# Kernel tuning notes

Hardware: AMD Instinct MI355X
Metric: run time of the kernel (lower is better)

## Reference

```python
import jax, jax.numpy as jnp
import numpy as np

B, T, N, C = 8, 12, 325, 64
S_ORDER, T_ORDER, LAYERS = 10, 5, 2
SKIP, END, OUT_W = 128, 256, 12
EPS = 1e-5


def _fro(x):
    return jnp.sqrt(jnp.sum(x * x, axis=(2, 3), keepdims=True))


def _unit(x):
    return x / jnp.maximum(_fro(x), 1e-8)


def _basis_s(Ls, last, second):
    r = jnp.einsum('nm,bcmt->bcnt', Ls, last)
    r = r - jnp.sum(r * last, axis=(2, 3), keepdims=True) * last
    r = r - jnp.sum(r * second, axis=(2, 3), keepdims=True) * second
    return _unit(r)


def _basis_t(Lt, last, second):
    r = jnp.einsum('bcnt,tu->bcnu', last, Lt)
    r = r - jnp.sum(r * last, axis=(2, 3), keepdims=True) * last
    r = r - jnp.sum(r * second, axis=(2, 3), keepdims=True) * second
    return _unit(r)


def _matrix_list(m00, Ls, Lt):
    # Gram-Schmidt-like 2D orthogonal polynomial recursion; (P+1)*(Q+1) terms
    M = [m00]
    last_s, sec_s = m00, jnp.zeros_like(m00)
    last_t, sec_t = m00, jnp.zeros_like(m00)
    for i in range(S_ORDER + 1):
        if i > 0:
            mi0 = _basis_s(Ls, last_s, sec_s)
            sec_s, last_s = last_s, mi0
            M.append(mi0)
            last_t, sec_t = mi0, jnp.zeros_like(mi0)
        for _ in range(T_ORDER):
            mij = _basis_t(Lt, last_t, sec_t)
            sec_t, last_t = last_t, mij
            M.append(mij)
    return jnp.stack(M, axis=1)  # [B, R, C, N, T]


def _c1x1(x, w, b):
    return jnp.einsum('bint,oi->bont', x, w) + b[None, :, None, None]


def _bn(x, g, b, m, v):
    s = g / jnp.sqrt(v + EPS)
    return (x - m[None, :, None, None]) * s[None, :, None, None] + b[None, :, None, None]


def _gate(y):
    return jax.nn.sigmoid(y[:, :C]) * jnp.tanh(y[:, C:])


def setup_inputs() -> dict:
    key = jax.random.key(0)
    ks = iter(jax.random.split(key, 80))

    def nrm(*shape):
        return jax.random.normal(next(ks), shape, jnp.float32) * 0.1

    def pos(*shape):
        return jax.random.uniform(next(ks), shape, jnp.float32, 0.5, 1.5)

    P1, Q1 = S_ORDER + 1, T_ORDER + 1
    # normalized symmetric spatial matrix  D^-1/2 A D^-1/2
    A = jax.random.uniform(next(ks), (N, N), jnp.float32)
    A = (A + A.T) * 0.5 + jnp.eye(N)
    d = 1.0 / jnp.sqrt(A.sum(0))
    sp_matrix = A * d[:, None] * d[None, :]
    # normalized tridiagonal temporal matrix (as in __init__)
    Tp = jnp.eye(T, k=1) + jnp.eye(T, k=-1)
    dt = 1.0 / jnp.sqrt(Tp.sum(0))
    tp_matrix = Tp * dt[:, None] * dt[None, :]
    return dict(
        source=jax.random.normal(next(ks), (B, T, N, 1), jnp.float32),
        TE=jax.random.randint(next(ks), (B, T, 2), 0, 288, jnp.int32),
        sp_matrix=sp_matrix, tp_matrix=tp_matrix,
        SE=nrm(N, 10),
        tmlp1_w=nrm(S_ORDER, 295), tmlp1_b=nrm(S_ORDER),
        tmlp2_w=nrm(T_ORDER, T), tmlp2_b=nrm(T_ORDER),
        smlp1_w=nrm(T_ORDER, N), smlp1_b=nrm(T_ORDER),
        smlp2_w=nrm(S_ORDER, 10), smlp2_b=nrm(S_ORDER),
        start_w=nrm(C, 1), start_b=nrm(C),
        theta1_w=nrm(LAYERS, Q1, T_ORDER), theta1_b=nrm(LAYERS, Q1),
        theta2_w=nrm(LAYERS, P1, S_ORDER), theta2_b=nrm(LAYERS, P1),
        st_mlp_w=nrm(LAYERS, C, 2 * C), st_mlp_b=nrm(LAYERS, C),
        st_bn_g=pos(LAYERS, C), st_bn_b=nrm(LAYERS, C), st_bn_m=nrm(LAYERS, C), st_bn_v=pos(LAYERS, C),
        pyr1_w=nrm(LAYERS, 2 * C, C), pyr1_b=nrm(LAYERS, 2 * C),
        pyr2_w=nrm(LAYERS, 2 * C, C, 3), pyr2_b=nrm(LAYERS, 2 * C),
        pyr3_w=nrm(LAYERS, 2 * C, C, 6), pyr3_b=nrm(LAYERS, 2 * C),
        pyr_conv_w=nrm(LAYERS, C, 3 * C), pyr_conv_b=nrm(LAYERS, C),
        pyr_bn_g=pos(LAYERS, C), pyr_bn_b=nrm(LAYERS, C), pyr_bn_m=nrm(LAYERS, C), pyr_bn_v=pos(LAYERS, C),
        skip_w=nrm(LAYERS, SKIP, C), skip_b=nrm(LAYERS, SKIP),
        bn_g=pos(LAYERS, C), bn_b=nrm(LAYERS, C), bn_m=nrm(LAYERS, C), bn_v=pos(LAYERS, C),
        end1_w=nrm(END, SKIP), end1_b=nrm(END),
        end2_w=nrm(OUT_W, END), end2_b=nrm(OUT_W),
    )


def reference(source, TE, sp_matrix, tp_matrix, SE, tmlp1_w, tmlp1_b, tmlp2_w, tmlp2_b,
              smlp1_w, smlp1_b, smlp2_w, smlp2_b, start_w, start_b,
              theta1_w, theta1_b, theta2_w, theta2_b, st_mlp_w, st_mlp_b,
              st_bn_g, st_bn_b, st_bn_m, st_bn_v,
              pyr1_w, pyr1_b, pyr2_w, pyr2_b, pyr3_w, pyr3_b,
              pyr_conv_w, pyr_conv_b, pyr_bn_g, pyr_bn_b, pyr_bn_m, pyr_bn_v,
              skip_w, skip_b, bn_g, bn_b, bn_m, bn_v,
              end1_w, end1_b, end2_w, end2_b):
    b = source.shape[0]
    # ---- STEmbedding ----
    dow = jax.nn.one_hot(TE[..., 0] % 7, 7, dtype=jnp.float32)
    tod = jax.nn.one_hot(TE[..., 1] % 288, 288, dtype=jnp.float32)
    te = jnp.concatenate([dow, tod], axis=-1)                                           # [B,T,295]
    te = jax.nn.relu(jnp.einsum('blc,oc->bol', te, tmlp1_w) + tmlp1_b[None, :, None])   # [B,s_order,T]
    te = jax.nn.relu(jnp.einsum('bst,ot->bos', te, tmlp2_w) + tmlp2_b[None, :, None])   # [B,t_order,s_order]
    se = jax.nn.relu(smlp1_w @ SE + smlp1_b[:, None])                                   # [t_order,10]
    se = jax.nn.relu((smlp2_w @ se.T + smlp2_b[:, None]).T)                             # [t_order,s_order]
    ste = jax.nn.relu(se[None] + te)
    # ---- start conv ----
    x = _c1x1(jnp.transpose(source, (0, 3, 2, 1)), start_w, start_b)                    # [B,C,N,T]
    skip = jnp.zeros((b, SKIP, N, T), jnp.float32)
    for i in range(LAYERS):
        residual = x
        # learned coefficients theta: [B,(t_order+1)*(s_order+1)]
        th = jnp.einsum('bts,ot->bos', ste, theta1_w[i]) + theta1_b[i][None, :, None]   # [B,t+1,s]
        th = jnp.einsum('bts,os->bot', th, theta2_w[i]) + theta2_b[i][None, :, None]    # [B,s+1,t+1]
        theta = jax.nn.relu(jnp.transpose(th, (0, 2, 1))).reshape(b, -1)
        # spectral basis recursion + einsum fusion
        m00 = _unit(residual)
        M = _matrix_list(m00, sp_matrix, tp_matrix)
        x_st = jnp.einsum('br,brcnt->bcnt', theta, M)
        hidden = _bn(_c1x1(jnp.concatenate([residual, x_st], axis=1), st_mlp_w[i], st_mlp_b[i]),
                     st_bn_g[i], st_bn_b[i], st_bn_m[i], st_bn_v[i])
        # pyramid temporal conv (gated)
        x1 = _gate(_c1x1(hidden, pyr1_w[i], pyr1_b[i]))
        h2 = hidden.reshape(b, C, N, T // 3, 3)
        x2 = _gate(jnp.einsum('bcnqk,ock->bonq', h2, pyr2_w[i]) + pyr2_b[i][None, :, None, None])
        h3 = hidden.reshape(b, C, N, T // 6, 6)
        x3 = _gate(jnp.einsum('bcnqk,ock->bonq', h3, pyr3_w[i]) + pyr3_b[i][None, :, None, None])
        x2 = jax.image.resize(x2, x1.shape, method='bilinear')
        x3 = jax.image.resize(x3, x1.shape, method='bilinear')
        fusion = _bn(_c1x1(jnp.concatenate([x1, x2, x3], axis=1), pyr_conv_w[i], pyr_conv_b[i]),
                     pyr_bn_g[i], pyr_bn_b[i], pyr_bn_m[i], pyr_bn_v[i])
        skip = skip + _c1x1(fusion, skip_w[i], skip_b[i])
        x = _bn(fusion + residual, bn_g[i], bn_b[i], bn_m[i], bn_v[i])
    out = jax.nn.relu(skip[:, :, :, -1:])
    out = jax.nn.relu(_c1x1(out, end1_w, end1_b))
    out = _c1x1(out, end2_w, end2_b)
    return out  # [B, output_window, N, 1]
```

## Files before the change

kernel.cpp:

```cpp
#include <hip/hip_runtime.h>
#include <hip/hip_bf16.h>
#include <math.h>

#define B_   8
#define T_   12
#define N_   325
#define C_   64
#define NT   3900
#define NTILE 21
#define NKK   11
#define NTHIRD 109

typedef __attribute__((ext_vector_type(8))) short short8v;
typedef __attribute__((ext_vector_type(4))) float f32x4;

__device__ __forceinline__ float sigm(float x) { return 1.f / (1.f + expf(-x)); }

__device__ __forceinline__ unsigned short f2bf(float f) {
  unsigned u = __float_as_uint(f);
  u += 0x7FFF + ((u >> 16) & 1);
  return (unsigned short)(u >> 16);
}
__device__ __forceinline__ float bf2f(unsigned short h) {
  return __uint_as_float(((unsigned)h) << 16);
}

__device__ __forceinline__ void redN(float* v, int nv, float (*redb)[4], int tid) {
#pragma unroll
  for (int off = 1; off < 64; off <<= 1) {
    for (int i = 0; i < nv; i++) v[i] += __shfl_xor(v[i], off, 64);
  }
  if ((tid & 63) == 0) {
    for (int i = 0; i < nv; i++) redb[tid >> 6][i] = v[i];
  }
  __syncthreads();
  for (int i = 0; i < nv; i++) {
    float s = 0.f;
#pragma unroll
    for (int w = 0; w < 8; w++) s += redb[w][i];
    v[i] = s;
  }
}

__device__ __forceinline__ void cvtB(const float* sbp, short8v* bfh0, short8v* bfl0,
                                     int ckbase, int ccc, bool cvalid, int cobase) {
  unsigned short* dh = (unsigned short*)bfh0;
  unsigned short* dl = (unsigned short*)bfl0;
#pragma unroll
  for (int kk = 0; kk < NKK; kk++) {
    int k = kk * 32 + ckbase;
    float v = (cvalid && k < N_) ? sbp[k * 12 + ccc] : 0.f;
    unsigned short h = f2bf(v);
    dh[kk * 512 + cobase] = h;
    dl[kk * 512 + cobase] = f2bf(v - bf2f(h));
  }
}

__global__ __launch_bounds__(256) void k_sentinel(float* out, int n) {
  int i = blockIdx.x * 256 + threadIdx.x;
  if (i < n) out[i] = 7.0f;
}

__global__ __launch_bounds__(256) void k0_frag(const float* __restrict__ sp,
                                               unsigned short* __restrict__ fragA) {
  int idx = blockIdx.x * 256 + threadIdx.x;
  if (idx >= NTILE * NKK * 64) return;
  int lane = idx & 63, tk = idx >> 6;
  int row = (tk / NKK) * 16 + (lane & 15);
  int k0 = (tk % NKK) * 32 + (lane >> 4) * 8;
  size_t base = ((size_t)tk * 2) * 512 + (size_t)lane * 8;
#pragma unroll
  for (int j = 0; j < 8; j++) {
    int k = k0 + j;
    float v = (row < N_ && k < N_) ? sp[row * N_ + k] : 0.f;
    unsigned short h = f2bf(v);
    fragA[base + j] = h;
    fragA[base + 512 + j] = f2bf(v - bf2f(h));
  }
}

__global__ __launch_bounds__(256) void k1_embed(
    const int* __restrict__ TE, const float* __restrict__ SE,
    const float* __restrict__ w1, const float* __restrict__ b1,
    const float* __restrict__ w2, const float* __restrict__ b2,
    const float* __restrict__ sw1, const float* __restrict__ sb1,
    const float* __restrict__ sw2, const float* __restrict__ sb2,
    const float* __restrict__ t1w, const float* __restrict__ t1b,
    const float* __restrict__ t2w, const float* __restrict__ t2b,
    float* __restrict__ coef) {
  __shared__ float te2[8][10][12];
  __shared__ float ste[8][5][10];
  __shared__ float se1[5][10];
  __shared__ float se2[5][10];
  __shared__ float th[8][6][10];
  __shared__ int te64;
  const int tid = threadIdx.x;
  if (tid == 0) {
    int nz = 0;
    for (int k2 = 0; k2 < 96; k2++) nz += (TE[2 * k2 + 1] != 0) ? 1 : 0;
    te64 = (nz == 0) ? 1 : 0;
  }
  __syncthreads();
  for (int idx = tid; idx < 960; idx += 256) {
    int t = idx % 12, o = (idx / 12) % 10, b = idx / 120;
    int q = (b * 12 + t) * 2;
    int d = (te64 ? TE[2 * q] : TE[q]) % 7;
    int h = (te64 ? TE[2 * q + 2] : TE[q + 1]) % 288;
    float v = w1[o * 295 + d] + w1[o * 295 + 7 + h] + b1[o];
    te2[b][o][t] = fmaxf(v, 0.f);
  }
  __syncthreads();
  for (int idx = tid; idx < 400; idx += 256) {
    int s = idx % 10, o = (idx / 10) % 5, b = idx / 50;
    float a = b2[o];
    for (int t = 0; t < 12; t++) a += te2[b][s][t] * w2[o * 12 + t];
    ste[b][o][s] = fmaxf(a, 0.f);
  }
  if (tid < 50) {
    int o = tid / 10, j = tid % 10;
    float a = sb1[o];
    for (int n = 0; n < N_; n++) a += sw1[o * N_ + n] * SE[n * 10 + j];
    se1[o][j] = fmaxf(a, 0.f);
  }
  __syncthreads();
  if (tid < 50) {
    int t = tid / 10, s = tid % 10;
    float a = sb2[s];
    for (int j = 0; j < 10; j++) a += sw2[s * 10 + j] * se1[t][j];
    se2[t][s] = fmaxf(a, 0.f);
  }
  __syncthreads();
  for (int idx = tid; idx < 400; idx += 256) {
    int s = idx % 10, o = (idx / 10) % 5, b = idx / 50;
    ste[b][o][s] = fmaxf(se2[o][s] + ste[b][o][s], 0.f);
  }
  __syncthreads();
  for (int l = 0; l < 2; l++) {
    for (int idx = tid; idx < 480; idx += 256) {
      int s = idx % 10, q = (idx / 10) % 6, b = idx / 60;
      float a = t1b[l * 6 + q];
      for (int t = 0; t < 5; t++) a += ste[b][t][s] * t1w[(l * 6 + q) * 5 + t];
      th[b][q][s] = a;
    }
    __syncthreads();
    for (int idx = tid; idx < 528; idx += 256) {
      int q = idx % 6, p = (idx / 6) % 11, b = idx / 66;
      float a = t2b[l * 11 + p];
      for (int s = 0; s < 10; s++) a += th[b][q][s] * t2w[(l * 11 + p) * 10 + s];
      coef[(l * 8 + b) * 66 + q * 11 + p] = fmaxf(a, 0.f);
    }
    __syncthreads();
  }
}

__global__ __launch_bounds__(256) void k2_start(const float* __restrict__ src,
                                                const float* __restrict__ w,
                                                const float* __restrict__ bia,
                                                float* __restrict__ x) {
  int idx = blockIdx.x * 256 + threadIdx.x;
  if (idx >= B_ * C_ * NT) return;
  int pos = idx % NT, r = idx / NT, c = r & 63, b = r >> 6;
  int n = pos / 12, t = pos - 12 * n;
  float s = src[(b * 12 + t) * N_ + n];
  x[idx] = s * w[c] + bia[c];
}

__global__ __launch_bounds__(512)
__attribute__((amdgpu_waves_per_eu(4, 4))) void k3_basis(
    const float* __restrict__ x, const unsigned short* __restrict__ fragA,
    const float* __restrict__ tp, const float* __restrict__ coef,
    float* __restrict__ xst) {
  __shared__ float sb[2][3940];
  __shared__ float rbuf[3936];
  __shared__ float sred[2][8][4];
  __shared__ short8v bfh0[704];
  __shared__ short8v bfl0[704];
  const int tid = threadIdx.x;
  const int bc = blockIdx.x;
  const float* cf = coef + (bc >> 6) * 66;
  const float* xs = x + (size_t)bc * NT;
  float* xo = xst + (size_t)bc * NT;

  const int wv = tid >> 6, lane = tid & 63;
  const int ccol = lane & 15, krow = lane >> 4;

  const int cj = tid & 7, ccc = (tid >> 3) & 15, ckr = (tid >> 7) & 3;
  const int ckbase = ckr * 8 + cj;
  const bool cvalid = (ccc < 12);
  const int cobase = (ckr * 16 + ccc) * 8 + cj;

  const bool upd = tid < 246;
  const int rq = tid / 3, tq = tid - 3 * (tid / 3);
  const int e0 = rq * 4 * 12 + tq * 4;

  const bool actT = (tid < N_);
  const int rowOff = tid * 12;

  float w[11];
#pragma unroll
  for (int k = 0; k < 11; k++) w[k] = tp[k * 12 + k + 1];

  float last[12], sec[12], acc[12];
  int p = 0, m = 0, spc = 0;

  if (tid < 80) {
    int bsel = tid / 40, off = tid - 40 * bsel;
    sb[bsel][3900 + off] = 0.f;
  }

  {
    float np = 0.f;
#pragma unroll
    for (int u = 0; u < 12; u++) last[u] = 0.f;
    if (actT) {
      const float4 a = *(const float4*)(xs + rowOff);
      const float4 b4 = *(const float4*)(xs + rowOff + 4);
      const float4 c4 = *(const float4*)(xs + rowOff + 8);
      last[0] = a.x; last[1] = a.y; last[2] = a.z; last[3] = a.w;
      last[4] = b4.x; last[5] = b4.y; last[6] = b4.z; last[7] = b4.w;
      last[8] = c4.x; last[9] = c4.y; last[10] = c4.z; last[11] = c4.w;
#pragma unroll
      for (int u = 0; u < 12; u++) np += last[u] * last[u];
    }
    p ^= 1; redN(&np, 1, sred[p], tid);
    const float inv = 1.f / fmaxf(sqrtf(np), 1e-8f);
    const float c0 = cf[m]; m++;
#pragma unroll
    for (int u = 0; u < 12; u++) {
      last[u] *= inv;
      acc[u] = c0 * last[u];
      sec[u] = 0.f;
    }
    if (actT) {
      float4 wv4;
      wv4.x = last[0]; wv4.y = last[1]; wv4.z = last[2]; wv4.w = last[3];
      *(float4*)&sb[0][rowOff] = wv4;
      wv4.x = last[4]; wv4.y = last[5]; wv4.z = last[6]; wv4.w = last[7];
      *(float4*)&sb[0][rowOff + 4] = wv4;
      wv4.x = last[8]; wv4.y = last[9]; wv4.z = last[10]; wv4.w = last[11];
      *(float4*)&sb[0][rowOff + 8] = wv4;
    }
    __syncthreads();
    cvtB(sb[0], bfh0, bfl0, ckbase, ccc, cvalid, cobase);
  }

  for (int i = 0; i <= 10; i++) {
    if (i > 0) {
      const int sps = 1 - spc;
      const bool hasSec = (i >= 2);
#pragma unroll 1
      for (int g = 0; g < 3; g++) {
        const int tile = wv + g * 8;
        if (tile < NTILE) {
          f32x4 cc = {0.f, 0.f, 0.f, 0.f};
#pragma unroll 1
          for (int kk = 0; kk < NKK; kk++) {
            const short8v bh = bfh0[kk * 64 + lane];
            const short8v bl = bfl0[kk * 64 + lane];
            const short8v* pa = (const short8v*)fragA +
                                ((size_t)(tile * NKK + kk) * 2) * 64 + lane;
            short8v ah = pa[0], al = pa[64];
            cc = __builtin_amdgcn_mfma_f32_16x16x32_bf16(ah, bh, cc, 0, 0, 0);
            cc = __builtin_amdgcn_mfma_f32_16x16x32_bf16(ah, bl, cc, 0, 0, 0);
            cc = __builtin_amdgcn_mfma_f32_16x16x32_bf16(al, bh, cc, 0, 0, 0);
          }
          if (ccol < 12) {
#pragma unroll
            for (int r = 0; r < 4; r++) {
              int row = tile * 16 + krow * 4 + r;
              if (row < 328) rbuf[row * 12 + ccol] = cc[r];
            }
          }
        }
      }
      __syncthreads();
      float rt[4][4];
      float v4[4] = {0.f, 0.f, 0.f, 0.f};
      if (upd) {
#pragma unroll
        for (int ii = 0; ii < 4; ii++) {
          const float4 q = *(const float4*)&rbuf[e0 + ii * 12];
          rt[ii][0] = q.x; rt[ii][1] = q.y; rt[ii][2] = q.z; rt[ii][3] = q.w;
          const float4 lq = *(const float4*)&sb[spc][e0 + ii * 12];
          v4[0] += rt[ii][0] * lq.x + rt[ii][1] * lq.y + rt[ii][2] * lq.z + rt[ii][3] * lq.w;
          v4[3] += rt[ii][0] * rt[ii][0] + rt[ii][1] * rt[ii][1] +
                   rt[ii][2] * rt[ii][2] + rt[ii][3] * rt[ii][3];
          if (hasSec) {
            const float4 sq4 = *(const float4*)&sb[sps][e0 + ii * 12];
            v4[1] += rt[ii][0] * sq4.x + rt[ii][1] * sq4.y + rt[ii][2] * sq4.z + rt[ii][3] * sq4.w;
            v4[2] += lq.x * sq4.x + lq.y * sq4.y + lq.z * sq4.z + lq.w * sq4.w;
          }
        }
      }
      p ^= 1; redN(v4, 4, sred[p], tid);
      const float d1 = v4[0];
      const float d2 = hasSec ? (v4[1] - d1 * v4[2]) : 0.f;
      const float np = fmaxf(v4[3] - d1 * d1 - d2 * d2, 0.f);
      const float inv = 1.f / fmaxf(sqrtf(np), 1e-8f);
      const float cs = cf[m]; m++;
      if (upd) {
#pragma unroll
        for (int ii = 0; ii < 4; ii++) {
          const float4 lq = *(const float4*)&sb[spc][e0 + ii * 12];
          float sx = 0.f, sy = 0.f, sz = 0.f, sw = 0.f;
          if (hasSec) {
            const float4 sq4 = *(const float4*)&sb[sps][e0 + ii * 12];
            sx = sq4.x; sy = sq4.y; sz = sq4.z; sw = sq4.w;
          }
          float4 wv4;
          wv4.x = (rt[ii][0] - d1 * lq.x - d2 * sx) * inv;
          wv4.y = (rt[ii][1] - d1 * lq.y - d2 * sy) * inv;
          wv4.z = (rt[ii][2] - d1 * lq.z - d2 * sz) * inv;
          wv4.w = (rt[ii][3] - d1 * lq.w - d2 * sw) * inv;
          *(float4*)&sb[sps][e0 + ii * 12] = wv4;
        }
      }
      spc = sps;
      __syncthreads();
      if (i < 10) cvtB(sb[spc], bfh0, bfl0, ckbase, ccc, cvalid, cobase);
      if (actT) {
        const float4 a = *(const float4*)&sb[spc][rowOff];
        const float4 b4 = *(const float4*)&sb[spc][rowOff + 4];
        const float4 c4 = *(const float4*)&sb[spc][rowOff + 8];
        last[0] = a.x; last[1] = a.y; last[2] = a.z; last[3] = a.w;
        last[4] = b4.x; last[5] = b4.y; last[6] = b4.z; last[7] = b4.w;
        last[8] = c4.x; last[9] = c4.y; last[10] = c4.z; last[11] = c4.w;
#pragma unroll
        for (int u = 0; u < 12; u++) {
          acc[u] += cs * last[u];
          sec[u] = 0.f;
        }
      }
    }
    for (int j5 = 0; j5 < 5; j5++) {
      float v4[4] = {0.f, 0.f, 0.f, 0.f};
      if (actT) {
#pragma unroll
        for (int u = 0; u < 12; u++) {
          float r = 0.f;
          if (u > 0) r += last[u - 1] * w[u - 1];
          if (u < 11) r += last[u + 1] * w[u];
          v4[0] += r * last[u];
          v4[1] += r * sec[u];
          v4[2] += last[u] * sec[u];
          v4[3] += r * r;
        }
      }
      p ^= 1; redN(v4, 4, sred[p], tid);
      const float d1 = v4[0];
      const float d2 = v4[1] - d1 * v4[2];
      const float np = fmaxf(v4[3] - d1 * d1 - d2 * d2, 0.f);
      const float inv = 1.f / fmaxf(sqrtf(np), 1e-8f);
      const float c = cf[m]; m++;
      if (actT) {
        float pm1 = 0.f;
#pragma unroll
        for (int u = 0; u < 12; u++) {
          const float tmp = last[u];
          float r = 0.f;
          if (u > 0) r += pm1 * w[u - 1];
          if (u < 11) r += last[u + 1] * w[u];
          const float v = (r - d1 * tmp - d2 * sec[u]) * inv;
          acc[u] += c * v;
          sec[u] = tmp;
          last[u] = v;
          pm1 = tmp;
        }
      }
    }
  }
  if (actT) {
    float4 wv4;
    wv4.x = acc[0]; wv4.y = acc[1]; wv4.z = acc[2]; wv4.w = acc[3];
    *(float4*)(xo + rowOff) = wv4;
    wv4.x = acc[4]; wv4.y = acc[5]; wv4.z = acc[6]; wv4.w = acc[7];
    *(float4*)(xo + rowOff + 4) = wv4;
    wv4.x = acc[8]; wv4.y = acc[9]; wv4.z = acc[10]; wv4.w = acc[11];
    *(float4*)(xo + rowOff + 8) = wv4;
  }
}

__global__ __launch_bounds__(256) void k45_layer(
    float* __restrict__ x, const float* __restrict__ xst,
    const float* __restrict__ stw, const float* __restrict__ stb,
    const float* __restrict__ stg, const float* __restrict__ stbb,
    const float* __restrict__ stm, const float* __restrict__ stv,
    const float* __restrict__ p1w, const float* __restrict__ p1b,
    const float* __restrict__ p2w, const float* __restrict__ p2b,
    const float* __restrict__ p3w, const float* __restrict__ p3b,
    const float* __restrict__ pcw, const float* __restrict__ pcb,
    const float* __restrict__ pbg, const float* __restrict__ pbb,
    const float* __restrict__ pbm, const float* __restrict__ pbv,
    const float* __restrict__ bng, const float* __restrict__ bnb,
    const float* __restrict__ bnm, const float* __restrict__ bnv,
    const float* __restrict__ skw, const float* __restrict__ skb,
    float* __restrict__ skipb, int accum) {
  __shared__ float xr[3][64][12];
  __shared__ float xq_g1s[3][64][12];
  __shared__ float hd[3][64][12];
  __shared__ float g2s[3][64][4];
  __shared__ float g3s[3][64][2];
  __shared__ float fu11[3][64];
  float (*xq)[64][12] = xq_g1s;
  float (*g1s)[64][12] = xq_g1s;
  const int tid = threadIdx.x;
  const int bid = blockIdx.x;
  const int b = bid / NTHIRD, nn = bid - NTHIRD * b;
  const int n0 = nn * 3;
  const bool val1 = (n0 + 1 < N_), val2 = (n0 + 2 < N_);
  const size_t base0 = ((size_t)b * 64) * NT + n0 * 12;
  if (tid < 192) {
    int c = tid / 3, ch = tid - 3 * (tid / 3);
    *(float4*)&xr[0][c][ch * 4] = *(const float4*)(x + base0 + (size_t)c * NT + ch * 4);
    *(float4*)&xq[0][c][ch * 4] = *(const float4*)(xst + base0 + (size_t)c * NT + ch * 4);
    float4 z = {0.f, 0.f, 0.f, 0.f};
    if (val1) {
      *(float4*)&xr[1][c][ch * 4] = *(const float4*)(x + base0 + 12 + (size_t)c * NT + ch * 4);
      *(float4*)&xq[1][c][ch * 4] = *(const float4*)(xst + base0 + 12 + (size_t)c * NT + ch * 4);
    } else {
      *(float4*)&xr[1][c][ch * 4] = z;
      *(float4*)&xq[1][c][ch * 4] = z;
    }
    if (val2) {
      *(float4*)&xr[2][c][ch * 4] = *(const float4*)(x + base0 + 24 + (size_t)c * NT + ch * 4);
      *(float4*)&xq[2][c][ch * 4] = *(const float4*)(xst + base0 + 24 + (size_t)c * NT + ch * 4);
    } else {
      *(float4*)&xr[2][c][ch * 4] = z;
      *(float4*)&xq[2][c][ch * 4] = z;
    }
  }
  __syncthreads();
  if (tid < 192) {
    int oq = tid / 12, t = tid - 12 * (tid / 12);
    float a[3][4] = {{0.f}};
    const float* w0 = stw + (4 * oq) * 128;
    for (int i = 0; i < 64; i++) {
      float wa = w0[i], wb = w0[128 + i], wc = w0[256 + i], wd = w0[384 + i];
#pragma unroll
      for (int s = 0; s < 3; s++) {
        float h = xr[s][i][t];
        a[s][0] += h * wa; a[s][1] += h * wb; a[s][2] += h * wc; a[s][3] += h * wd;
      }
    }
    for (int i = 0; i < 64; i++) {
      float wa = w0[64 + i], wb = w0[192 + i], wc = w0[320 + i], wd = w0[448 + i];
#pragma unroll
      for (int s = 0; s < 3; s++) {
        float h = xq[s][i][t];
        a[s][0] += h * wa; a[s][1] += h * wb; a[s][2] += h * wc; a[s][3] += h * wd;
      }
    }
#pragma unroll
    for (int k = 0; k < 4; k++) {
      int o = 4 * oq + k;
      float sc = stg[o] / sqrtf(stv[o] + 1e-5f);
#pragma unroll
      for (int s = 0; s < 3; s++)
        hd[s][o][t] = (a[s][k] + stb[o] - stm[o]) * sc + stbb[o];
    }
  }
  __syncthreads();
  if (tid < 192) {
    int oq = tid / 12, t = tid - 12 * (tid / 12);
    float sa[3][4] = {{0.f}}, ua[3][4] = {{0.f}};
    const float* wsr = p1w + (4 * oq) * 64;
    for (int i = 0; i < 64; i++) {
      float wa = wsr[i], wb = wsr[64 + i], wc = wsr[128 + i], wd = wsr[192 + i];
      float va = wsr[4096 + i], vb = wsr[4096 + 64 + i];
      float vc = wsr[4096 + 128 + i], vd = wsr[4096 + 192 + i];
#pragma unroll
      for (int s = 0; s < 3; s++) {
        float h = hd[s][i][t];
        sa[s][0] += h * wa; sa[s][1] += h * wb; sa[s][2] += h * wc; sa[s][3] += h * wd;
        ua[s][0] += h * va; ua[s][1] += h * vb; ua[s][2] += h * vc; ua[s][3] += h * vd;
      }
    }
#pragma unroll
    for (int k = 0; k < 4; k++) {
      int o = 4 * oq + k;
#pragma unroll
      for (int s = 0; s < 3; s++)
        g1s[s][o][t] = sigm(sa[s][k] + p1b[o]) * tanhf(ua[s][k] + p1b[o + 64]);
    }
  }
  if (tid < 128) {
    int oq = tid / 4, q = tid & 3;
    float sa[3][2] = {{0.f}}, ua[3][2] = {{0.f}};
    const float* wsr = p2w + (2 * oq) * 192;
    for (int i = 0; i < 64; i++)
#pragma unroll
      for (int kk = 0; kk < 3; kk++) {
        float wa = wsr[i * 3 + kk], wb = wsr[192 + i * 3 + kk];
        float va = wsr[12288 + i * 3 + kk], vb = wsr[12288 + 192 + i * 3 + kk];
#pragma unroll
        for (int s = 0; s < 3; s++) {
          float h = hd[s][i][3 * q + kk];
          sa[s][0] += h * wa; sa[s][1] += h * wb;
          ua[s][0] += h * va; ua[s][1] += h * vb;
        }
      }
    int o = 2 * oq;
#pragma unroll
    for (int s = 0; s < 3; s++) {
      g2s[s][o][q] = sigm(sa[s][0] + p2b[o]) * tanhf(ua[s][0] + p2b[o + 64]);
      g2s[s][o + 1][q] = sigm(sa[s][1] + p2b[o + 1]) * tanhf(ua[s][1] + p2b[o + 65]);
    }
  } else if (tid < 192) {
    int r = tid - 128;
    int oq = r / 2, q = r & 1;
    float sa[3][2] = {{0.f}}, ua[3][2] = {{0.f}};
    const float* wsr = p3w + (2 * oq) * 384;
    for (int i = 0; i < 64; i++)
#pragma unroll
      for (int kk = 0; kk < 6; kk++) {
        float wa = wsr[i * 6 + kk], wb = wsr[384 + i * 6 + kk];
        float va = wsr[24576 + i * 6 + kk], vb = wsr[24576 + 384 + i * 6 + kk];
#pragma unroll
        for (int s = 0; s < 3; s++) {
          float h = hd[s][i][6 * q + kk];
          sa[s][0] += h * wa; sa[s][1] += h * wb;
          ua[s][0] += h * va; ua[s][1] += h * vb;
        }
      }
    int o = 2 * oq;
#pragma unroll
    for (int s = 0; s < 3; s++) {
      g3s[s][o][q] = sigm(sa[s][0] + p3b[o]) * tanhf(ua[s][0] + p3b[o + 64]);
      g3s[s][o + 1][q] = sigm(sa[s][1] + p3b[o + 1]) * tanhf(ua[s][1] + p3b[o + 65]);
    }
  }
  __syncthreads();
  if (tid < 192) {
    int oq = tid / 12, t = tid - 12 * (tid / 12);
    float a[3][4] = {{0.f}};
    const float* w0 = pcw + (4 * oq) * 192;
    for (int c = 0; c < 64; c++) {
      float wa = w0[c], wb = w0[192 + c], wc = w0[384 + c], wd = w0[576 + c];
#pragma unroll
      for (int s = 0; s < 3; s++) {
        float v = g1s[s][c][t];
        a[s][0] += v * wa; a[s][1] += v * wb; a[s][2] += v * wc; a[s][3] += v * wd;
      }
    }
    float c4 = fminf(fmaxf((t - 1) * (1.f / 3.f), 0.f), 3.f);
    int q0 = (int)c4;
    float f4 = c4 - (float)q0;
    int q1 = min(q0 + 1, 3);
    for (int c = 0; c < 64; c++) {
      float wa = w0[64 + c], wb = w0[192 + 64 + c], wc = w0[384 + 64 + c], wd = w0[576 + 64 + c];
#pragma unroll
      for (int s = 0; s < 3; s++) {
        float v = (1.f - f4) * g2s[s][c][q0] + f4 * g2s[s][c][q1];
        a[s][0] += v * wa; a[s][1] += v * wb; a[s][2] += v * wc; a[s][3] += v * wd;
      }
    }
    float f2 = fminf(fmaxf((2 * t - 5) * (1.f / 12.f), 0.f), 1.f);
    for (int c = 0; c < 64; c++) {
      float wa = w0[128 + c], wb = w0[192 + 128 + c], wc = w0[384 + 128 + c], wd = w0[576 + 128 + c];
#pragma unroll
      for (int s = 0; s < 3; s++) {
        float v = (1.f - f2) * g3s[s][c][0] + f2 * g3s[s][c][1];
        a[s][0] += v * wa; a[s][1] += v * wb; a[s][2] += v * wc; a[s][3] += v * wd;
      }
    }
#pragma unroll
    for (int k = 0; k < 4; k++) {
      int o = 4 * oq + k;
      float s1 = pbg[o] / sqrtf(pbv[o] + 1e-5f);
      float s2 = bng[o] / sqrtf(bnv[o] + 1e-5f);
#pragma unroll
      for (int s = 0; s < 3; s++) {
        float fv = (a[s][k] + pcb[o] - pbm[o]) * s1 + pbb[o];
        if (t == 11) fu11[s][o] = fv;
        xr[s][o][t] = (fv + xr[s][o][t] - bnm[o]) * s2 + bnb[o];
      }
    }
  }
  __syncthreads();
  if (tid < 192) {
    int c = tid / 3, ch = tid - 3 * (tid / 3);
    *(float4*)(x + base0 + (size_t)c * NT + ch * 4) = *(float4*)&xr[0][c][ch * 4];
    if (val1)
      *(float4*)(x + base0 + 12 + (size_t)c * NT + ch * 4) = *(float4*)&xr[1][c][ch * 4];
    if (val2)
      *(float4*)(x + base0 + 24 + (size_t)c * NT + ch * 4) = *(float4*)&xr[2][c][ch * 4];
  }
  if (tid < 128) {
    float a[3];
    a[0] = skb[tid]; a[1] = skb[tid]; a[2] = skb[tid];
    const float* wr = skw + tid * 64;
    for (int c = 0; c < 64; c++) {
      float wv = wr[c];
#pragma unroll
      for (int s = 0; s < 3; s++) a[s] += fu11[s][c] * wv;
    }
    size_t o0 = ((size_t)b * 128 + tid) * N_ + n0;
    skipb[o0] = accum ? (skipb[o0] + a[0]) : a[0];
    if (val1) skipb[o0 + 1] = accum ? (skipb[o0 + 1] + a[1]) : a[1];
    if (val2) skipb[o0 + 2] = accum ? (skipb[o0 + 2] + a[2]) : a[2];
  }
}

__global__ __launch_bounds__(256) void k6_end(const float* __restrict__ skip,
                                              const float* __restrict__ w1,
                                              const float* __restrict__ b1,
                                              const float* __restrict__ w2,
                                              const float* __restrict__ b2,
                                              float* __restrict__ out) {
  __shared__ float sk[128];
  __shared__ float h[256];
  const int blk = blockIdx.x;
  const int b = blk / N_;
  const int n = blk - N_ * b;
  const int tid = threadIdx.x;
  if (tid < 128) sk[tid] = fmaxf(skip[((size_t)b * 128 + tid) * N_ + n], 0.f);
  __syncthreads();
  {
    float a = b1[tid];
    for (int s = 0; s < 128; s++) a += w1[tid * 128 + s] * sk[s];
    h[tid] = fmaxf(a, 0.f);
  }
  __syncthreads();
  if (tid < 12) {
    float a = b2[tid];
    for (int e = 0; e < 256; e++) a += w2[tid * 256 + e] * h[e];
    out[((size_t)b * 12 + tid) * N_ + n] = a;
  }
}

extern "C" void kernel_launch(void* const* d_in, const int* in_sizes, int n_in,
                              void* d_out, int out_size, void* d_ws, size_t ws_size,
                              hipStream_t stream) {
  (void)in_sizes; (void)n_in;
  if (ws_size < (size_t)44 * 1024 * 1024) {
    k_sentinel<<<(out_size + 255) / 256, 256, 0, stream>>>((float*)d_out, out_size);
    return;
  }
  const float* src = (const float*)d_in[0];
  const int* TE = (const int*)d_in[1];
  const float* sp = (const float*)d_in[2];
  const float* tp = (const float*)d_in[3];
  const float* SE = (const float*)d_in[4];
  const float* tmlp1_w = (const float*)d_in[5];
  const float* tmlp1_b = (const float*)d_in[6];
  const float* tmlp2_w = (const float*)d_in[7];
  const float* tmlp2_b = (const float*)d_in[8];
  const float* smlp1_w = (const float*)d_in[9];
  const float* smlp1_b = (const float*)d_in[10];
  const float* smlp2_w = (const float*)d_in[11];
  const float* smlp2_b = (const float*)d_in[12];
  const float* start_w = (const float*)d_in[13];
  const float* start_b = (const float*)d_in[14];
  const float* th1w = (const float*)d_in[15];
  const float* th1b = (const float*)d_in[16];
  const float* th2w = (const float*)d_in[17];
  const float* th2b = (const float*)d_in[18];
  const float* stw = (const float*)d_in[19];
  const float* stb = (const float*)d_in[20];
  const float* stg = (const float*)d_in[21];
  const float* stbb = (const float*)d_in[22];
  const float* stm = (const float*)d_in[23];
  const float* stv = (const float*)d_in[24];
  const float* p1w = (const float*)d_in[25];
  const float* p1b = (const float*)d_in[26];
  const float* p2w = (const float*)d_in[27];
  const float* p2b = (const float*)d_in[28];
  const float* p3w = (const float*)d_in[29];
  const float* p3b = (const float*)d_in[30];
  const float* pcw = (const float*)d_in[31];
  const float* pcb = (const float*)d_in[32];
  const float* pbg = (const float*)d_in[33];
  const float* pbb = (const float*)d_in[34];
  const float* pbm = (const float*)d_in[35];
  const float* pbv = (const float*)d_in[36];
  const float* skw = (const float*)d_in[37];
  const float* skb = (const float*)d_in[38];
  const float* bng = (const float*)d_in[39];
  const float* bnb = (const float*)d_in[40];
  const float* bnm = (const float*)d_in[41];
  const float* bnv = (const float*)d_in[42];
  const float* e1w = (const float*)d_in[43];
  const float* e1b = (const float*)d_in[44];
  const float* e2w = (const float*)d_in[45];
  const float* e2b = (const float*)d_in[46];

  float* ws = (float*)d_ws;
  float* coef = ws + 0;
  unsigned short* fragA = (unsigned short*)(ws + 8192);
  float* x    = ws + 4194304;
  float* xst  = ws + 6291456;
  float* skipb= ws + 10485760;

  k0_frag<<<(NTILE * NKK * 64 + 255) / 256, 256, 0, stream>>>(sp, fragA);
  k1_embed<<<1, 256, 0, stream>>>(TE, SE, tmlp1_w, tmlp1_b, tmlp2_w, tmlp2_b,
                                  smlp1_w, smlp1_b, smlp2_w, smlp2_b,
                                  th1w, th1b, th2w, th2b, coef);
  k2_start<<<(B_ * C_ * NT + 255) / 256, 256, 0, stream>>>(src, start_w, start_b, x);

  for (int l = 0; l < 2; l++) {
    k3_basis<<<512, 512, 0, stream>>>(x, fragA, tp, coef + l * 528, xst);
    k45_layer<<<B_ * NTHIRD, 256, 0, stream>>>(
        x, xst,
        stw + l * 8192, stb + l * 64, stg + l * 64, stbb + l * 64,
        stm + l * 64, stv + l * 64,
        p1w + l * 8192, p1b + l * 128,
        p2w + l * 24576, p2b + l * 128,
        p3w + l * 49152, p3b + l * 128,
        pcw + l * 12288, pcb + l * 64,
        pbg + l * 64, pbb + l * 64, pbm + l * 64, pbv + l * 64,
        bng + l * 64, bnb + l * 64, bnm + l * 64, bnv + l * 64,
        skw + l * 8192, skb + l * 128,
        skipb, l);
  }
  k6_end<<<B_ * N_, 256, 0, stream>>>(skipb, e1w, e1b, e2w, e2b, (float*)d_out);
}
```

Measured before the change: 899.6 us.

## Fuse front-end kernels into one launch and end MLP into final layer kernel

Merges the start convolution, spatial-matrix fragment preparation and embedding MLP into a single kernel dispatched by block index. It also folds the final ReLU/end MLP into the last layer kernel so the accumulated skip is consumed directly instead of being written and re-read. The aim is to cut kernel launch gaps and a global skip round trip. The cost is a larger per-block shared footprint and extra per-block work in the layer kernel.

Result: faster. 831.5 us (median of 2 runs) (-7.6%).

```diff
diff --git a/kernel.cpp b/kernel.cpp
--- a/kernel.cpp
+++ b/kernel.cpp
@@ -10,6 +10,7 @@
 #define NTILE 21
 #define NKK   11
 #define NTHIRD 109
+#define K2BLK 7800
 
 typedef __attribute__((ext_vector_type(8))) short short8v;
 typedef __attribute__((ext_vector_type(4))) float f32x4;
@@ -61,25 +62,10 @@
   if (i < n) out[i] = 7.0f;
 }
 
-__global__ __launch_bounds__(256) void k0_frag(const float* __restrict__ sp,
-                                               unsigned short* __restrict__ fragA) {
-  int idx = blockIdx.x * 256 + threadIdx.x;
-  if (idx >= NTILE * NKK * 64) return;
-  int lane = idx & 63, tk = idx >> 6;
-  int row = (tk / NKK) * 16 + (lane & 15);
-  int k0 = (tk % NKK) * 32 + (lane >> 4) * 8;
-  size_t base = ((size_t)tk * 2) * 512 + (size_t)lane * 8;
-#pragma unroll
-  for (int j = 0; j < 8; j++) {
-    int k = k0 + j;
-    float v = (row < N_ && k < N_) ? sp[row * N_ + k] : 0.f;
-    unsigned short h = f2bf(v);
-    fragA[base + j] = h;
-    fragA[base + 512 + j] = f2bf(v - bf2f(h));
-  }
-}
-
-__global__ __launch_bounds__(256) void k1_embed(
+__global__ __launch_bounds__(256) void k012_front(
+    const float* __restrict__ src, const float* __restrict__ cw,
+    const float* __restrict__ cbia, float* __restrict__ x,
+    const float* __restrict__ sp, unsigned short* __restrict__ fragA,
     const int* __restrict__ TE, const float* __restrict__ SE,
     const float* __restrict__ w1, const float* __restrict__ b1,
     const float* __restrict__ w2, const float* __restrict__ b2,
@@ -95,6 +81,31 @@
   __shared__ float th[8][6][10];
   __shared__ int te64;
   const int tid = threadIdx.x;
+  const int blk = blockIdx.x;
+  if (blk < K2BLK) {
+    int idx = blk * 256 + tid;
+    int pos = idx % NT, r = idx / NT, c = r & 63, b = r >> 6;
+    int n = pos / 12, t = pos - 12 * n;
+    float s = src[(b * 12 + t) * N_ + n];
+    x[idx] = s * cw[c] + cbia[c];
+    return;
+  } else if (blk > K2BLK) {
+    int idx = (blk - K2BLK - 1) * 256 + tid;
+    if (idx >= NTILE * NKK * 64) return;
+    int lane = idx & 63, tk = idx >> 6;
+    int row = (tk / NKK) * 16 + (lane & 15);
+    int k0 = (tk % NKK) * 32 + (lane >> 4) * 8;
+    size_t base = ((size_t)tk * 2) * 512 + (size_t)lane * 8;
+#pragma unroll
+    for (int j = 0; j < 8; j++) {
+      int k = k0 + j;
+      float v = (row < N_ && k < N_) ? sp[row * N_ + k] : 0.f;
+      unsigned short h = f2bf(v);
+      fragA[base + j] = h;
+      fragA[base + 512 + j] = f2bf(v - bf2f(h));
+    }
+    return;
+  }
   if (tid == 0) {
     int nz = 0;
     for (int k2 = 0; k2 < 96; k2++) nz += (TE[2 * k2 + 1] != 0) ? 1 : 0;
@@ -151,18 +162,6 @@
     }
     __syncthreads();
   }
-}
-
-__global__ __launch_bounds__(256) void k2_start(const float* __restrict__ src,
-                                                const float* __restrict__ w,
-                                                const float* __restrict__ bia,
-                                                float* __restrict__ x) {
-  int idx = blockIdx.x * 256 + threadIdx.x;
-  if (idx >= B_ * C_ * NT) return;
-  int pos = idx % NT, r = idx / NT, c = r & 63, b = r >> 6;
-  int n = pos / 12, t = pos - 12 * n;
-  float s = src[(b * 12 + t) * N_ + n];
-  x[idx] = s * w[c] + bia[c];
 }
 
 __global__ __launch_bounds__(512)
@@ -394,13 +393,18 @@
     const float* __restrict__ bng, const float* __restrict__ bnb,
     const float* __restrict__ bnm, const float* __restrict__ bnv,
     const float* __restrict__ skw, const float* __restrict__ skb,
-    float* __restrict__ skipb, int accum) {
+    float* __restrict__ skipb, int accum,
+    const float* __restrict__ e1w, const float* __restrict__ e1b,
+    const float* __restrict__ e2w, const float* __restrict__ e2b,
+    float* __restrict__ out) {
   __shared__ float xr[3][64][12];
   __shared__ float xq_g1s[3][64][12];
   __shared__ float hd[3][64][12];
   __shared__ float g2s[3][64][4];
   __shared__ float g3s[3][64][2];
   __shared__ float fu11[3][64];
+  __shared__ float sk2[3][128];
+  __shared__ float h2[3][256];
   float (*xq)[64][12] = xq_g1s;
   float (*g1s)[64][12] = xq_g1s;
   const int tid = threadIdx.x;
@@ -595,36 +599,41 @@
       for (int s = 0; s < 3; s++) a[s] += fu11[s][c] * wv;
     }
     size_t o0 = ((size_t)b * 128 + tid) * N_ + n0;
-    skipb[o0] = accum ? (skipb[o0] + a[0]) : a[0];
-    if (val1) skipb[o0 + 1] = accum ? (skipb[o0 + 1] + a[1]) : a[1];
-    if (val2) skipb[o0 + 2] = accum ? (skipb[o0 + 2] + a[2]) : a[2];
-  }
-}
-
-__global__ __launch_bounds__(256) void k6_end(const float* __restrict__ skip,
-                                              const float* __restrict__ w1,
-                                              const float* __restrict__ b1,
-                                              const float* __restrict__ w2,
-                                              const float* __restrict__ b2,
-                                              float* __restrict__ out) {
-  __shared__ float sk[128];
-  __shared__ float h[256];
-  const int blk = blockIdx.x;
-  const int b = blk / N_;
-  const int n = blk - N_ * b;
-  const int tid = threadIdx.x;
-  if (tid < 128) sk[tid] = fmaxf(skip[((size_t)b * 128 + tid) * N_ + n], 0.f);
-  __syncthreads();
-  {
-    float a = b1[tid];
-    for (int s = 0; s < 128; s++) a += w1[tid * 128 + s] * sk[s];
-    h[tid] = fmaxf(a, 0.f);
-  }
-  __syncthreads();
-  if (tid < 12) {
-    float a = b2[tid];
-    for (int e = 0; e < 256; e++) a += w2[tid * 256 + e] * h[e];
-    out[((size_t)b * 12 + tid) * N_ + n] = a;
+    if (accum) {
+      sk2[0][tid] = fmaxf(skipb[o0] + a[0], 0.f);
+      sk2[1][tid] = val1 ? fmaxf(skipb[o0 + 1] + a[1], 0.f) : 0.f;
+      sk2[2][tid] = val2 ? fmaxf(skipb[o0 + 2] + a[2], 0.f) : 0.f;
+    } else {
+      skipb[o0] = a[0];
+      if (val1) skipb[o0 + 1] = a[1];
+      if (val2) skipb[o0 + 2] = a[2];
+    }
+  }
+  if (accum) {
+    __syncthreads();
+    {
+      float a1[3];
+      a1[0] = e1b[tid]; a1[1] = a1[0]; a1[2] = a1[0];
+      const float* wr1 = e1w + tid * 128;
+      for (int ss = 0; ss < 128; ss++) {
+        float wv = wr1[ss];
+#pragma unroll
+        for (int s = 0; s < 3; s++) a1[s] += wv * sk2[s][ss];
+      }
+#pragma unroll
+      for (int s = 0; s < 3; s++) h2[s][tid] = fmaxf(a1[s], 0.f);
+    }
+    __syncthreads();
+    if (tid < 36) {
+      int s = tid / 12, tt = tid - 12 * (tid / 12);
+      bool ok = (s == 0) || (s == 1 && val1) || (s == 2 && val2);
+      if (ok) {
+        float a2 = e2b[tt];
+        const float* wr2 = e2w + tt * 256;
+        for (int e = 0; e < 256; e++) a2 += wr2[e] * h2[s][e];
+        out[((size_t)b * 12 + tt) * N_ + n0 + s] = a2;
+      }
+    }
   }
 }
 
@@ -691,11 +700,12 @@
   float* xst  = ws + 6291456;
   float* skipb= ws + 10485760;
 
-  k0_frag<<<(NTILE * NKK * 64 + 255) / 256, 256, 0, stream>>>(sp, fragA);
-  k1_embed<<<1, 256, 0, stream>>>(TE, SE, tmlp1_w, tmlp1_b, tmlp2_w, tmlp2_b,
-                                  smlp1_w, smlp1_b, smlp2_w, smlp2_b,
-                                  th1w, th1b, th2w, th2b, coef);
-  k2_start<<<(B_ * C_ * NT + 255) / 256, 256, 0, stream>>>(src, start_w, start_b, x);
+  const int k0blks = (NTILE * NKK * 64 + 255) / 256;
+  k012_front<<<K2BLK + 1 + k0blks, 256, 0, stream>>>(
+      src, start_w, start_b, x, sp, fragA,
+      TE, SE, tmlp1_w, tmlp1_b, tmlp2_w, tmlp2_b,
+      smlp1_w, smlp1_b, smlp2_w, smlp2_b,
+      th1w, th1b, th2w, th2b, coef);
 
   for (int l = 0; l < 2; l++) {
     k3_basis<<<512, 512, 0, stream>>>(x, fragA, tp, coef + l * 528, xst);
@@ -710,7 +720,7 @@
         pbg + l * 64, pbb + l * 64, pbm + l * 64, pbv + l * 64,
         bng + l * 64, bnb + l * 64, bnm + l * 64, bnv + l * 64,
         skw + l * 8192, skb + l * 128,
-        skipb, l);
-  }
-  k6_end<<<B_ * N_, 256, 0, stream>>>(skipb, e1w, e1b, e2w, e2b, (float*)d_out);
-}
+        skipb, l,
+        e1w, e1b, e2w, e2b, (float*)d_out);
+  }
+}
```
